# Optimization experiments

Measured on AMD Instinct MI355X. Metric: run time of the kernel, lower is better.

## Reference

```python
import jax, jax.numpy as jnp
import numpy as np
import math

TOKEN_DIM = 1024
NUM_HEADS = 16
HEAD_DIM = TOKEN_DIM // NUM_HEADS
T, B, N = 32, 32, 64


def setup_inputs() -> dict:
    key = jax.random.key(0)
    ks = jax.random.split(key, 9)
    query_vec = jax.random.normal(ks[0], (T, B, TOKEN_DIM), dtype=jnp.float32)
    tokens = jax.random.normal(ks[1], (T, B, N, TOKEN_DIM), dtype=jnp.float32)
    gate_logits = jax.random.normal(ks[2], (T, B, N), dtype=jnp.float32)
    scale = 1.0 / math.sqrt(TOKEN_DIM)
    Wq = jax.random.normal(ks[3], (TOKEN_DIM, TOKEN_DIM), dtype=jnp.float32) * scale
    Wk = jax.random.normal(ks[4], (TOKEN_DIM, TOKEN_DIM), dtype=jnp.float32) * scale
    Wv = jax.random.normal(ks[5], (TOKEN_DIM, TOKEN_DIM), dtype=jnp.float32) * scale
    bq = jnp.zeros((TOKEN_DIM,), dtype=jnp.float32)
    bk = jnp.zeros((TOKEN_DIM,), dtype=jnp.float32)
    bv = jnp.zeros((TOKEN_DIM,), dtype=jnp.float32)
    return {"query_vec": query_vec, "tokens": tokens, "gate_logits": gate_logits,
            "Wq": Wq, "bq": bq, "Wk": Wk, "bk": bk, "Wv": Wv, "bv": bv}


def reference(query_vec, tokens, gate_logits, Wq, bq, Wk, bk, Wv, bv):
    # QKV projections
    q = query_vec @ Wq + bq                      # [T,B,D]
    k = tokens @ Wk + bk                         # [T,B,N,D]
    v = tokens @ Wv + bv                         # [T,B,N,D]
    q = q.reshape(T, B, NUM_HEADS, HEAD_DIM)
    k = k.reshape(T, B, N, NUM_HEADS, HEAD_DIM)
    v = v.reshape(T, B, N, NUM_HEADS, HEAD_DIM)
    logits = jnp.einsum('tbhd,tbnhd->tbhn', q, k) / math.sqrt(HEAD_DIM)
    logits = logits + gate_logits[:, :, None, :]
    attn = jax.nn.softmax(logits, axis=-1)       # [T,B,H,N]
    attended = jnp.einsum('tbhn,tbnhd->tbhd', attn, v)
    attended = attended.reshape(T, B, TOKEN_DIM)
    mean_attn = attn.mean(axis=2)                # [T,B,N]
    return (attended, mean_attn, logits)
```

## Files before the change

### kernel.cpp

```cpp
#include <hip/hip_runtime.h>
#include <hip/hip_bf16.h>
#include <hip/hip_cooperative_groups.h>

namespace cg = cooperative_groups;

typedef __attribute__((ext_vector_type(4))) float f32x4;
typedef __attribute__((ext_vector_type(8))) short bf16x8;
typedef unsigned int u32;
typedef unsigned short u16;

#define DEV static __device__ __forceinline__


DEV u16 f2bf(float x){
  union { float f; u32 u; } v; v.f = x;
  u32 r = v.u + 0x7FFFu + ((v.u >> 16) & 1u);
  return (u16)(r >> 16);
}
DEV float bf2f(u16 s){
  union { u32 u; float f; } v; v.u = ((u32)s) << 16;
  return v.f;
}

#define MFMA16(a,b,c) __builtin_amdgcn_mfma_f32_16x16x32_bf16((a),(b),(c),0,0,0)

DEV int tok_off(int n, int dbyte){ return n*2048 + (dbyte ^ ((n & 7) << 4)); }

#define MEGA_DYN_LDS 65536

__global__ __launch_bounds__(256, 2) void k_mega(
    const float* __restrict__ qv, const float* __restrict__ tokens,
    const float* __restrict__ gate,
    const float* __restrict__ Wq, const float* __restrict__ bq,
    const float* __restrict__ Wk, const float* __restrict__ bk,
    const float* __restrict__ Wv, const float* __restrict__ bv,
    u16* __restrict__ qvB, u16* __restrict__ WqT, u16* __restrict__ WkB,
    u16* __restrict__ WvT, float* __restrict__ qf, u16* __restrict__ qb,
    u16* __restrict__ U, u16* __restrict__ ctxb,
    float* __restrict__ out_att, float* __restrict__ out_mean,
    float* __restrict__ out_logits){
  extern __shared__ __align__(16) char smem[];
  __shared__ __align__(16) char sstat[10496];
  cg::grid_group grid = cg::this_grid();
  const int tid = threadIdx.x;
  const int bx  = blockIdx.x;
  const int l = tid & 63, w = tid >> 6, g = l >> 4, li = l & 15;

  {
    const f32x4* s4 = (const f32x4*)qv;
    uint2* d2 = (uint2*)qvB;
    int g0 = bx*256 + tid;
    #pragma unroll
    for (int i = 0; i < 2; ++i){
      int idx = g0 + i*131072;
      f32x4 v = s4[idx];
      uint2 pk;
      pk.x = (u32)f2bf(v.x) | ((u32)f2bf(v.y) << 16);
      pk.y = (u32)f2bf(v.z) | ((u32)f2bf(v.w) << 16);
      d2[idx] = pk;
    }
  }
  {
    u16 (*tile)[65] = (u16 (*)[65])sstat;
    for (int tl = bx; tl < 768; tl += 512){
      __syncthreads();
      const int which = tl >> 8, t8 = tl & 255;
      const float* src = which==0 ? Wq : (which==1 ? Wk : Wv);
      const int bi = (t8 >> 4) << 6, bj = (t8 & 15) << 6;
      #pragma unroll
      for (int k2 = 0; k2 < 16; ++k2){
        int e = tid + (k2 << 8); int r = e >> 6, c = e & 63;
        tile[r][c] = f2bf(src[(size_t)(bi + r)*1024 + bj + c]);
      }
      __syncthreads();
      if (which == 1){
        #pragma unroll
        for (int k2 = 0; k2 < 16; ++k2){
          int e = tid + (k2 << 8); int r = e >> 6, c = e & 63;
          WkB[(size_t)(bi + r)*1024 + bj + c] = tile[r][c];
        }
      } else {
        u16* dst = which==0 ? WqT : WvT;
        #pragma unroll
        for (int k2 = 0; k2 < 16; ++k2){
          int e = tid + (k2 << 8); int r = e >> 6, c = e & 63;
          dst[(size_t)(bj + r)*1024 + bi + c] = tile[c][r];
        }
      }
    }
  }
  __threadfence(); grid.sync(); __threadfence();

  {
    const int wm = w & 1, wn = w >> 1;
    const int m_base = (bx >> 5)*64 + wm*32;
    const int n_base = (bx & 31)*32 + wn*16;
    f32x4 acc[2]; acc[0] = (f32x4)0.0f; acc[1] = (f32x4)0.0f;
    #pragma unroll 4
    for (int kb = 0; kb < 32; ++kb){
      const int k0 = kb*32 + g*8;
      bf16x8 b = *(const bf16x8*)(WqT + (size_t)(n_base + li)*1024 + k0);
      #pragma unroll
      for (int rt = 0; rt < 2; ++rt){
        bf16x8 a = *(const bf16x8*)(qvB + (size_t)(m_base + rt*16 + li)*1024 + k0);
        acc[rt] = MFMA16(a, b, acc[rt]);
      }
    }
    #pragma unroll
    for (int rt = 0; rt < 2; ++rt)
      #pragma unroll
      for (int r = 0; r < 4; ++r){
        int m = m_base + rt*16 + g*4 + r;
        int n = n_base + li;
        float val = acc[rt][r] + bq[n];
        qf[(size_t)m*1024 + n] = val;
        qb[(size_t)m*1024 + n] = f2bf(val);
      }
  }
  __threadfence(); grid.sync(); __threadfence();

  {
    u16 (*stile)[64] = (u16 (*)[64])sstat;
    const int wm = w & 1, wn = w >> 1;
    for (int i = 0; i < 8; ++i){
      const int tl = bx*8 + i;
      const int tb0 = (tl >> 8)*64, d0 = ((tl >> 4) & 15)*64, h = tl & 15;
      f32x4 acc[2][2];
      #pragma unroll
      for (int a0=0;a0<2;++a0)
        #pragma unroll
        for (int b0=0;b0<2;++b0) acc[a0][b0] = (f32x4)0.0f;
      #pragma unroll
      for (int kb = 0; kb < 2; ++kb){
        const int k0 = h*64 + kb*32 + g*8;
        bf16x8 a[2], b[2];
        #pragma unroll
        for (int rt=0;rt<2;++rt)
          a[rt] = *(const bf16x8*)(qb + (size_t)(tb0 + wm*32 + rt*16 + li)*1024 + k0);
        #pragma unroll
        for (int ct=0;ct<2;++ct)
          b[ct] = *(const bf16x8*)(WkB + (size_t)(d0 + wn*32 + ct*16 + li)*1024 + k0);
        #pragma unroll
        for (int rt=0;rt<2;++rt)
          #pragma unroll
          for (int ct=0;ct<2;++ct)
            acc[rt][ct] = MFMA16(a[rt], b[ct], acc[rt][ct]);
      }
      __syncthreads();
      #pragma unroll
      for (int rt=0;rt<2;++rt)
        #pragma unroll
        for (int ct=0;ct<2;++ct)
          #pragma unroll
          for (int r=0;r<4;++r)
            stile[wm*32 + rt*16 + g*4 + r][wn*32 + ct*16 + li] = f2bf(acc[rt][ct][r]);
      __syncthreads();
      const int rr = tid >> 2, cg4 = tid & 3;
      f32x4* dst = (f32x4*)(U + ((size_t)(tb0 + rr)*16 + h)*1024 + d0 + cg4*16);
      const f32x4* s4 = (const f32x4*)(&stile[rr][cg4*16]);
      dst[0] = s4[0]; dst[1] = s4[1];
    }
  }
  __threadfence(); grid.sync(); __threadfence();

  {
    float* part_s   = (float*)(sstat);
    float* logits_s = (float*)(sstat + 4096);
    float* p_s      = (float*)(sstat + 8192);
    float* csum     = (float*)(sstat + 10240);
    float* r_s      = (float*)(sstat + 10304);
    float* mzs      = (float*)(sstat + 10368);
    const int nt = w & 1, kh = w >> 1;
    const int sh = tid >> 4, sj = tid & 15;

    __syncthreads();
    for (int tbi = 0; tbi < 2; ++tbi){
      const int tb = bx + tbi*512;

      bf16x8 a[16];
      const bf16x8* Ub = (const bf16x8*)(U + (size_t)tb*16384);
      #pragma unroll
      for (int i = 0; i < 16; ++i)
        a[i] = Ub[li*128 + (kh*16 + i)*4 + g];

      {
        const float* qp = qf + (size_t)tb*1024 + sh*64 + sj*4;
        const float* bp = bk + sh*64 + sj*4;
        float part = qp[0]*bp[0] + qp[1]*bp[1] + qp[2]*bp[2] + qp[3]*bp[3];
        part += __shfl_xor(part, 1); part += __shfl_xor(part, 2);
        part += __shfl_xor(part, 4); part += __shfl_xor(part, 8);
        if (sj == 0) csum[sh] = part;
      }

      float m_run = -1e30f, z_run = 0.0f;
      f32x4 cacc[4][4];
      #pragma unroll
      for (int i=0;i<4;++i)
        #pragma unroll
        for (int j=0;j<4;++j) cacc[i][j] = (f32x4)0.0f;

      const f32x4* src4 = (const f32x4*)(tokens + (size_t)tb*65536);

      for (int c = 0; c < 2; ++c){
        const int n0 = c*32;
        __syncthreads();
        #pragma unroll 8
        for (int it = 0; it < 32; ++it){
          f32x4 v = src4[(size_t)(n0 + it)*256 + tid];
          uint2 pk;
          pk.x = (u32)f2bf(v.x) | ((u32)f2bf(v.y) << 16);
          pk.y = (u32)f2bf(v.z) | ((u32)f2bf(v.w) << 16);
          *(uint2*)(smem + tok_off(it, tid*8)) = pk;
        }
        __syncthreads();
        {
          f32x4 acc = (f32x4)0.0f;
          #pragma unroll
          for (int i = 0; i < 16; ++i){
            int kb = kh*16 + i;
            bf16x8 b = *(const bf16x8*)(smem + tok_off(nt*16 + li, (kb*32 + g*8)*2));
            acc = MFMA16(a[i], b, acc);
          }
          *(f32x4*)(part_s + (size_t)(w*64 + l)*4) = acc;
          __syncthreads();
          if (kh == 0){
            acc += *(const f32x4*)(part_s + (size_t)((w+2)*64 + l)*4);
            float gv = gate[(size_t)tb*64 + n0 + nt*16 + li];
            #pragma unroll
            for (int r = 0; r < 4; ++r){
              int h = g*4 + r;
              logits_s[h*64 + n0 + nt*16 + li] = (acc[r] + csum[h])*0.125f + gv;
            }
          }
          __syncthreads();
        }
        {
          float lv0 = logits_s[sh*64 + n0 + sj];
          float lv1 = logits_s[sh*64 + n0 + 16 + sj];
          out_logits[(size_t)tb*1024 + sh*64 + n0 + sj]      = lv0;
          out_logits[(size_t)tb*1024 + sh*64 + n0 + 16 + sj] = lv1;
          float cm = fmaxf(lv0, lv1);
          cm = fmaxf(cm, __shfl_xor(cm, 1)); cm = fmaxf(cm, __shfl_xor(cm, 2));
          cm = fmaxf(cm, __shfl_xor(cm, 4)); cm = fmaxf(cm, __shfl_xor(cm, 8));
          float m_new = fmaxf(m_run, cm);
          float rsc = __expf(m_run - m_new);
          float p0 = __expf(lv0 - m_new), p1 = __expf(lv1 - m_new);
          float zs = p0 + p1;
          zs += __shfl_xor(zs, 1); zs += __shfl_xor(zs, 2);
          zs += __shfl_xor(zs, 4); zs += __shfl_xor(zs, 8);
          z_run = z_run * rsc + zs;
          m_run = m_new;
          p_s[sj*16 + sh]        = p0;
          p_s[(sj + 16)*16 + sh] = p1;
          if (sj == 0){
            r_s[sh] = rsc;
            if (c == 1){ mzs[sh*2] = m_new; mzs[sh*2 + 1] = 1.0f / z_run; }
          }
        }
        __syncthreads();
        {
          float rr[4];
          #pragma unroll
          for (int hh = 0; hh < 4; ++hh) rr[hh] = r_s[w*4 + hh];
          #pragma unroll
          for (int dq = 0; dq < 4; ++dq)
            #pragma unroll
            for (int hh = 0; hh < 4; ++hh) cacc[dq][hh] *= rr[hh];
          for (int nl = 0; nl < 32; ++nl){
            f32x4 p = *(const f32x4*)(p_s + nl*16 + w*4);
            #pragma unroll
            for (int dq = 0; dq < 4; ++dq){
              uint2 t2 = *(const uint2*)(smem + tok_off(nl, (dq*256 + l*4)*2));
              float f0 = bf2f((u16)(t2.x & 0xFFFFu));
              float f1 = bf2f((u16)(t2.x >> 16));
              float f2 = bf2f((u16)(t2.y & 0xFFFFu));
              float f3 = bf2f((u16)(t2.y >> 16));
              #pragma unroll
              for (int hh = 0; hh < 4; ++hh){
                float av = p[hh];
                cacc[dq][hh].x += av*f0; cacc[dq][hh].y += av*f1;
                cacc[dq][hh].z += av*f2; cacc[dq][hh].w += av*f3;
              }
            }
          }
        }
      }

      if (tid < 64){
        float s = 0.0f;
        #pragma unroll
        for (int h = 0; h < 16; ++h)
          s += __expf(logits_s[h*64 + tid] - mzs[h*2]) * mzs[h*2 + 1];
        out_mean[(size_t)tb*64 + tid] = s * 0.0625f;
      }

      #pragma unroll
      for (int hh = 0; hh < 4; ++hh){
        const int h = w*4 + hh;
        const float zinv = mzs[h*2 + 1];
        #pragma unroll
        for (int dq = 0; dq < 4; ++dq){
          f32x4 v = cacc[dq][hh];
          uint2 pk;
          pk.x = (u32)f2bf(v.x * zinv) | ((u32)f2bf(v.y * zinv) << 16);
          pk.y = (u32)f2bf(v.z * zinv) | ((u32)f2bf(v.w * zinv) << 16);
          *(uint2*)(ctxb + ((size_t)tb*16 + h)*1024 + dq*256 + l*4) = pk;
        }
      }
      __syncthreads();
    }
  }
  __threadfence(); grid.sync(); __threadfence();

  {
    const int wm = w & 1, wn = w >> 1;
    const int m_base = (bx >> 4)*32, h = bx & 15;
    f32x4 acc[2]; acc[0] = (f32x4)0.0f; acc[1] = (f32x4)0.0f;
    #pragma unroll 4
    for (int kb = 0; kb < 32; ++kb){
      const int k0 = kb*32 + g*8;
      bf16x8 a = *(const bf16x8*)(ctxb + ((size_t)(m_base + wm*16 + li)*16 + h)*1024 + k0);
      #pragma unroll
      for (int ct = 0; ct < 2; ++ct){
        bf16x8 b = *(const bf16x8*)(WvT + (size_t)(h*64 + wn*32 + ct*16 + li)*1024 + k0);
        acc[ct] = MFMA16(a, b, acc[ct]);
      }
    }
    #pragma unroll
    for (int ct = 0; ct < 2; ++ct)
      #pragma unroll
      for (int r = 0; r < 4; ++r){
        int m = m_base + wm*16 + g*4 + r;
        int dout = h*64 + wn*32 + ct*16 + li;
        out_att[(size_t)m*1024 + dout] = acc[ct][r] + bv[dout];
      }
  }
}

__global__ __launch_bounds__(256) void k_convert(
    const float* __restrict__ Wq, const float* __restrict__ Wk, const float* __restrict__ Wv,
    u16* __restrict__ WqT, u16* __restrict__ WkB, u16* __restrict__ WvT){
  __shared__ u16 tile[64][65];
  const int which = blockIdx.y;
  const float* src = which==0 ? Wq : (which==1 ? Wk : Wv);
  const int bi = (blockIdx.x >> 4) << 6;
  const int bj = (blockIdx.x & 15) << 6;
  const int t  = threadIdx.x;
  #pragma unroll
  for (int k2 = 0; k2 < 16; ++k2){
    int e = t + (k2 << 8);
    int r = e >> 6, c = e & 63;
    tile[r][c] = f2bf(src[(size_t)(bi + r)*1024 + bj + c]);
  }
  __syncthreads();
  if (which == 1){
    #pragma unroll
    for (int k2 = 0; k2 < 16; ++k2){
      int e = t + (k2 << 8); int r = e >> 6, c = e & 63;
      WkB[(size_t)(bi + r)*1024 + bj + c] = tile[r][c];
    }
  } else {
    u16* dst = which==0 ? WqT : WvT;
    #pragma unroll
    for (int k2 = 0; k2 < 16; ++k2){
      int e = t + (k2 << 8); int r = e >> 6, c = e & 63;
      dst[(size_t)(bj + r)*1024 + bi + c] = tile[c][r];
    }
  }
}

__global__ __launch_bounds__(256) void k_qproj(
    const float* __restrict__ qv, const u16* __restrict__ WqT, const float* __restrict__ bq,
    float* __restrict__ qf, u16* __restrict__ qb){
  const int l = threadIdx.x & 63, w = threadIdx.x >> 6;
  const int wm = w & 1, wn = w >> 1;
  const int g = l >> 4, li = l & 15;
  const int m_base = blockIdx.x*64 + wm*32;
  const int n_base = blockIdx.y*64 + wn*32;
  f32x4 acc[2][2];
  #pragma unroll
  for (int i=0;i<2;++i)
    #pragma unroll
    for (int j=0;j<2;++j) acc[i][j] = (f32x4)0.0f;

  #pragma unroll 4
  for (int kb = 0; kb < 32; ++kb){
    const int k0 = kb*32 + g*8;
    bf16x8 a[2], b[2];
    #pragma unroll
    for (int rt = 0; rt < 2; ++rt){
      const float* p = qv + (size_t)(m_base + rt*16 + li)*1024 + k0;
      f32x4 lo = *(const f32x4*)p;
      f32x4 hi = *(const f32x4*)(p+4);
      union { u16 s[8]; bf16x8 v; } u;
      u.s[0]=f2bf(lo.x); u.s[1]=f2bf(lo.y); u.s[2]=f2bf(lo.z); u.s[3]=f2bf(lo.w);
      u.s[4]=f2bf(hi.x); u.s[5]=f2bf(hi.y); u.s[6]=f2bf(hi.z); u.s[7]=f2bf(hi.w);
      a[rt] = u.v;
    }
    #pragma unroll
    for (int ct = 0; ct < 2; ++ct)
      b[ct] = *(const bf16x8*)(WqT + (size_t)(n_base + ct*16 + li)*1024 + k0);
    #pragma unroll
    for (int rt = 0; rt < 2; ++rt)
      #pragma unroll
      for (int ct = 0; ct < 2; ++ct)
        acc[rt][ct] = MFMA16(a[rt], b[ct], acc[rt][ct]);
  }
  #pragma unroll
  for (int rt=0;rt<2;++rt)
    #pragma unroll
    for (int ct=0;ct<2;++ct)
      #pragma unroll
      for (int r=0;r<4;++r){
        int m = m_base + rt*16 + g*4 + r;
        int n = n_base + ct*16 + li;
        float val = acc[rt][ct][r] + bq[n];
        qf[(size_t)m*1024 + n] = val;
        qb[(size_t)m*1024 + n] = f2bf(val);
      }
}

__global__ __launch_bounds__(256) void k_umat(
    const u16* __restrict__ qb, const u16* __restrict__ WkB, u16* __restrict__ U){
  __shared__ __align__(16) u16 stile[64][64];
  const int l = threadIdx.x & 63, w = threadIdx.x >> 6;
  const int wm = w & 1, wn = w >> 1, g = l >> 4, li = l & 15;
  const int tb0 = blockIdx.x*64, d0 = blockIdx.y*64, h = blockIdx.z;
  f32x4 acc[2][2];
  #pragma unroll
  for (int i=0;i<2;++i)
    #pragma unroll
    for (int j=0;j<2;++j) acc[i][j] = (f32x4)0.0f;

  #pragma unroll
  for (int kb = 0; kb < 2; ++kb){
    const int k0 = h*64 + kb*32 + g*8;
    bf16x8 a[2], b[2];
    #pragma unroll
    for (int rt=0;rt<2;++rt)
      a[rt] = *(const bf16x8*)(qb + (size_t)(tb0 + wm*32 + rt*16 + li)*1024 + k0);
    #pragma unroll
    for (int ct=0;ct<2;++ct)
      b[ct] = *(const bf16x8*)(WkB + (size_t)(d0 + wn*32 + ct*16 + li)*1024 + k0);
    #pragma unroll
    for (int rt=0;rt<2;++rt)
      #pragma unroll
      for (int ct=0;ct<2;++ct)
        acc[rt][ct] = MFMA16(a[rt], b[ct], acc[rt][ct]);
  }
  #pragma unroll
  for (int rt=0;rt<2;++rt)
    #pragma unroll
    for (int ct=0;ct<2;++ct)
      #pragma unroll
      for (int r=0;r<4;++r)
        stile[wm*32 + rt*16 + g*4 + r][wn*32 + ct*16 + li] = f2bf(acc[rt][ct][r]);
  __syncthreads();
  const int r = threadIdx.x >> 2, cg4 = threadIdx.x & 3;
  f32x4* dst = (f32x4*)(U + ((size_t)(tb0 + r)*16 + h)*1024 + d0 + cg4*16);
  const f32x4* s4 = (const f32x4*)(&stile[r][cg4*16]);
  dst[0] = s4[0]; dst[1] = s4[1];
}

#define K3_LDS 76032
__global__ __launch_bounds__(256, 2) void k_attn(
    const float* __restrict__ tokens, const float* __restrict__ gate,
    const u16* __restrict__ U, const float* __restrict__ qf, const float* __restrict__ bk,
    float* __restrict__ out_logits, float* __restrict__ out_mean, u16* __restrict__ ctx){
  extern __shared__ __align__(16) char smem[];
  float* part_s   = (float*)(smem + 65536);
  float* logits_s = (float*)(smem + 69632);
  float* p_s      = (float*)(smem + 73728);
  float* csum     = (float*)(smem + 75776);
  float* r_s      = (float*)(smem + 75840);
  float* mzs      = (float*)(smem + 75904);
  const int tb = blockIdx.x;
  const int tid = threadIdx.x;
  const int l = tid & 63, w = tid >> 6, g = l >> 4, li = l & 15;
  const int nt = w & 1, kh = w >> 1;
  const int sh = tid >> 4, sj = tid & 15;

  bf16x8 a[16];
  const bf16x8* Ub = (const bf16x8*)(U + (size_t)tb*16384);
  #pragma unroll
  for (int i = 0; i < 16; ++i)
    a[i] = Ub[li*128 + (kh*16 + i)*4 + g];

  {
    const float* qp = qf + (size_t)tb*1024 + sh*64 + sj*4;
    const float* bp = bk + sh*64 + sj*4;
    float part = qp[0]*bp[0] + qp[1]*bp[1] + qp[2]*bp[2] + qp[3]*bp[3];
    part += __shfl_xor(part, 1); part += __shfl_xor(part, 2);
    part += __shfl_xor(part, 4); part += __shfl_xor(part, 8);
    if (sj == 0) csum[sh] = part;
  }

  float m_run = -1e30f, z_run = 0.0f;
  f32x4 cacc[4][4];
  #pragma unroll
  for (int i=0;i<4;++i)
    #pragma unroll
    for (int j=0;j<4;++j) cacc[i][j] = (f32x4)0.0f;

  const f32x4* src4 = (const f32x4*)(tokens + (size_t)tb*65536);

  for (int c = 0; c < 2; ++c){
    const int n0 = c*32;
    __syncthreads();
    #pragma unroll 8
    for (int it = 0; it < 32; ++it){
      f32x4 v = src4[(size_t)(n0 + it)*256 + tid];
      uint2 pk;
      pk.x = (u32)f2bf(v.x) | ((u32)f2bf(v.y) << 16);
      pk.y = (u32)f2bf(v.z) | ((u32)f2bf(v.w) << 16);
      *(uint2*)(smem + tok_off(it, tid*8)) = pk;
    }
    __syncthreads();
    {
      f32x4 acc = (f32x4)0.0f;
      #pragma unroll
      for (int i = 0; i < 16; ++i){
        int kb = kh*16 + i;
        bf16x8 b = *(const bf16x8*)(smem + tok_off(nt*16 + li, (kb*32 + g*8)*2));
        acc = MFMA16(a[i], b, acc);
      }
      *(f32x4*)(part_s + (size_t)(w*64 + l)*4) = acc;
      __syncthreads();
      if (kh == 0){
        acc += *(const f32x4*)(part_s + (size_t)((w+2)*64 + l)*4);
        float gv = gate[(size_t)tb*64 + n0 + nt*16 + li];
        #pragma unroll
        for (int r = 0; r < 4; ++r){
          int h = g*4 + r;
          logits_s[h*64 + n0 + nt*16 + li] = (acc[r] + csum[h])*0.125f + gv;
        }
      }
      __syncthreads();
    }
    {
      float lv0 = logits_s[sh*64 + n0 + sj];
      float lv1 = logits_s[sh*64 + n0 + 16 + sj];
      out_logits[(size_t)tb*1024 + sh*64 + n0 + sj]      = lv0;
      out_logits[(size_t)tb*1024 + sh*64 + n0 + 16 + sj] = lv1;
      float cm = fmaxf(lv0, lv1);
      cm = fmaxf(cm, __shfl_xor(cm, 1)); cm = fmaxf(cm, __shfl_xor(cm, 2));
      cm = fmaxf(cm, __shfl_xor(cm, 4)); cm = fmaxf(cm, __shfl_xor(cm, 8));
      float m_new = fmaxf(m_run, cm);
      float rsc = __expf(m_run - m_new);
      float p0 = __expf(lv0 - m_new), p1 = __expf(lv1 - m_new);
      float zs = p0 + p1;
      zs += __shfl_xor(zs, 1); zs += __shfl_xor(zs, 2);
      zs += __shfl_xor(zs, 4); zs += __shfl_xor(zs, 8);
      z_run = z_run * rsc + zs;
      m_run = m_new;
      p_s[sj*16 + sh]        = p0;
      p_s[(sj + 16)*16 + sh] = p1;
      if (sj == 0){
        r_s[sh] = rsc;
        if (c == 1){ mzs[sh*2] = m_new; mzs[sh*2 + 1] = 1.0f / z_run; }
      }
    }
    __syncthreads();
    {
      float rr[4];
      #pragma unroll
      for (int hh = 0; hh < 4; ++hh) rr[hh] = r_s[w*4 + hh];
      #pragma unroll
      for (int dq = 0; dq < 4; ++dq)
        #pragma unroll
        for (int hh = 0; hh < 4; ++hh) cacc[dq][hh] *= rr[hh];
      for (int nl = 0; nl < 32; ++nl){
        f32x4 p = *(const f32x4*)(p_s + nl*16 + w*4);
        #pragma unroll
        for (int dq = 0; dq < 4; ++dq){
          uint2 t2 = *(const uint2*)(smem + tok_off(nl, (dq*256 + l*4)*2));
          float f0 = bf2f((u16)(t2.x & 0xFFFFu));
          float f1 = bf2f((u16)(t2.x >> 16));
          float f2 = bf2f((u16)(t2.y & 0xFFFFu));
          float f3 = bf2f((u16)(t2.y >> 16));
          #pragma unroll
          for (int hh = 0; hh < 4; ++hh){
            float av = p[hh];
            cacc[dq][hh].x += av*f0; cacc[dq][hh].y += av*f1;
            cacc[dq][hh].z += av*f2; cacc[dq][hh].w += av*f3;
          }
        }
      }
    }
  }

  if (tid < 64){
    float s = 0.0f;
    #pragma unroll
    for (int h = 0; h < 16; ++h)
      s += __expf(logits_s[h*64 + tid] - mzs[h*2]) * mzs[h*2 + 1];
    out_mean[(size_t)tb*64 + tid] = s * 0.0625f;
  }

  #pragma unroll
  for (int hh = 0; hh < 4; ++hh){
    const int h = w*4 + hh;
    const float zinv = mzs[h*2 + 1];
    #pragma unroll
    for (int dq = 0; dq < 4; ++dq){
      f32x4 v = cacc[dq][hh];
      uint2 pk;
      pk.x = (u32)f2bf(v.x * zinv) | ((u32)f2bf(v.y * zinv) << 16);
      pk.y = (u32)f2bf(v.z * zinv) | ((u32)f2bf(v.w * zinv) << 16);
      *(uint2*)(ctx + ((size_t)tb*16 + h)*1024 + dq*256 + l*4) = pk;
    }
  }
}

__global__ __launch_bounds__(256) void k_attended(
    const u16* __restrict__ ctx, const u16* __restrict__ WvT, const float* __restrict__ bv,
    float* __restrict__ out_att){
  const int l = threadIdx.x & 63, w = threadIdx.x >> 6;
  const int wm = w & 1, wn = w >> 1, g = l >> 4, li = l & 15;
  const int tb0 = blockIdx.x*64, h = blockIdx.y;
  f32x4 acc[2][2];
  #pragma unroll
  for (int i=0;i<2;++i)
    #pragma unroll
    for (int j=0;j<2;++j) acc[i][j] = (f32x4)0.0f;

  #pragma unroll 4
  for (int kb = 0; kb < 32; ++kb){
    const int k0 = kb*32 + g*8;
    bf16x8 a[2], b[2];
    #pragma unroll
    for (int rt=0;rt<2;++rt)
      a[rt] = *(const bf16x8*)(ctx + ((size_t)(tb0 + wm*32 + rt*16 + li)*16 + h)*1024 + k0);
    #pragma unroll
    for (int ct=0;ct<2;++ct)
      b[ct] = *(const bf16x8*)(WvT + (size_t)(h*64 + wn*32 + ct*16 + li)*1024 + k0);
    #pragma unroll
    for (int rt=0;rt<2;++rt)
      #pragma unroll
      for (int ct=0;ct<2;++ct)
        acc[rt][ct] = MFMA16(a[rt], b[ct], acc[rt][ct]);
  }
  #pragma unroll
  for (int rt=0;rt<2;++rt)
    #pragma unroll
    for (int ct=0;ct<2;++ct)
      #pragma unroll
      for (int r=0;r<4;++r){
        int m = tb0 + wm*32 + rt*16 + g*4 + r;
        int dout = h*64 + wn*32 + ct*16 + li;
        out_att[(size_t)m*1024 + dout] = acc[rt][ct][r] + bv[dout];
      }
}

extern "C" void kernel_launch(void* const* d_in, const int* in_sizes, int n_in,
                              void* d_out, int out_size, void* d_ws, size_t ws_size,
                              hipStream_t stream){
  const float* qv     = (const float*)d_in[0];
  const float* tokens = (const float*)d_in[1];
  const float* gate   = (const float*)d_in[2];
  const float* Wq     = (const float*)d_in[3];
  const float* bq     = (const float*)d_in[4];
  const float* Wk     = (const float*)d_in[5];
  const float* bk     = (const float*)d_in[6];
  const float* Wv     = (const float*)d_in[7];
  const float* bv     = (const float*)d_in[8];

  char* ws = (char*)d_ws;
  u16*   qvB = (u16*)(ws);
  u16*   WqT = (u16*)(ws + (2u<<20));
  u16*   WkB = (u16*)(ws + (4u<<20));
  u16*   WvT = (u16*)(ws + (6u<<20));
  float* qf  = (float*)(ws + (8u<<20));
  u16*   qb  = (u16*)(ws + (12u<<20));
  u16*   U   = (u16*)(ws + (14u<<20));
  u16*   ctxb= (u16*)(ws + (46u<<20));

  float* out_att    = (float*)d_out;
  float* out_mean   = out_att + 1048576;
  float* out_logits = out_att + 1114112;

  int dev = 0; (void)hipGetDevice(&dev);
  int coop = 0; (void)hipDeviceGetAttribute(&coop, hipDeviceAttributeCooperativeLaunch, dev);
  int ncu = 0;  (void)hipDeviceGetAttribute(&ncu, hipDeviceAttributeMultiprocessorCount, dev);
  int perCU = 0;
  hipError_t oe = hipOccupancyMaxActiveBlocksPerMultiprocessor(
                      &perCU, (const void*)k_mega, 256, (size_t)MEGA_DYN_LDS);
  bool use_coop = (coop != 0) && (oe == hipSuccess) && ((long)perCU * (long)ncu >= 512);

  if (use_coop){
    void* args[] = { (void*)&qv, (void*)&tokens, (void*)&gate,
                     (void*)&Wq, (void*)&bq, (void*)&Wk, (void*)&bk,
                     (void*)&Wv, (void*)&bv,
                     (void*)&qvB, (void*)&WqT, (void*)&WkB, (void*)&WvT,
                     (void*)&qf, (void*)&qb, (void*)&U, (void*)&ctxb,
                     (void*)&out_att, (void*)&out_mean, (void*)&out_logits };
    hipError_t le = hipLaunchCooperativeKernel((const void*)k_mega, dim3(512), dim3(256),
                                               args, MEGA_DYN_LDS, stream);
    if (le == hipSuccess) return;
    use_coop = false;
  }

  (void)hipFuncSetAttribute((const void*)k_attn,
                            hipFuncAttributeMaxDynamicSharedMemorySize, K3_LDS);
  k_convert <<<dim3(256, 3),    256, 0,      stream>>>(Wq, Wk, Wv, WqT, WkB, WvT);
  k_qproj   <<<dim3(16, 16),    256, 0,      stream>>>(qv, WqT, bq, qf, qb);
  k_umat    <<<dim3(16, 16, 16),256, 0,      stream>>>(qb, WkB, U);
  k_attn    <<<dim3(1024),      256, K3_LDS, stream>>>(tokens, gate, U, qf, bk,
                                                       out_logits, out_mean, ctxb);
  k_attended<<<dim3(16, 16),    256, 0,      stream>>>(ctxb, WvT, bv, out_att);
}
```

Measured before the change: 177.1 us.

## Prefetch next token chunk into registers while computing softmax and context

Flattens the two-level (tb, chunk) loop in the attention phase into four rounds. Each round issues the global loads for the next 32-token chunk into a register staging array before the softmax and context accumulation, then converts it to bf16 and writes it into shared memory afterwards. The aim is to hide global-memory load latency of the token stream behind compute. The cost is 32 extra f32x4 registers of staging per thread, which may cause spills or lower occupancy in a cooperative kernel.

```diff
diff --git a/kernel.cpp b/kernel.cpp
--- a/kernel.cpp
+++ b/kernel.cpp
@@ -174,16 +174,35 @@
     const int sh = tid >> 4, sj = tid & 15;
 
     __syncthreads();
-    for (int tbi = 0; tbi < 2; ++tbi){
-      const int tb = bx + tbi*512;
-
-      bf16x8 a[16];
-      const bf16x8* Ub = (const bf16x8*)(U + (size_t)tb*16384);
-      #pragma unroll
-      for (int i = 0; i < 16; ++i)
-        a[i] = Ub[li*128 + (kh*16 + i)*4 + g];
-
-      {
+
+    {
+      const f32x4* src4 = (const f32x4*)(tokens + (size_t)bx*65536);
+      f32x4 pstg[32];
+      #pragma unroll
+      for (int it = 0; it < 32; ++it) pstg[it] = src4[(size_t)it*256 + tid];
+      #pragma unroll
+      for (int it = 0; it < 32; ++it){
+        f32x4 v = pstg[it];
+        uint2 pk;
+        pk.x = (u32)f2bf(v.x) | ((u32)f2bf(v.y) << 16);
+        pk.y = (u32)f2bf(v.z) | ((u32)f2bf(v.w) << 16);
+        *(uint2*)(smem + tok_off(it, tid*8)) = pk;
+      }
+    }
+
+    float m_run = -1e30f, z_run = 0.0f;
+    f32x4 cacc[4][4];
+
+    for (int r = 0; r < 4; ++r){
+      const int c = r & 1, n0 = c*32;
+      const int tb = bx + (r >> 1)*512;
+
+      if (c == 0){
+        m_run = -1e30f; z_run = 0.0f;
+        #pragma unroll
+        for (int i=0;i<4;++i)
+          #pragma unroll
+          for (int j=0;j<4;++j) cacc[i][j] = (f32x4)0.0f;
         const float* qp = qf + (size_t)tb*1024 + sh*64 + sj*4;
         const float* bp = bk + sh*64 + sj*4;
         float part = qp[0]*bp[0] + qp[1]*bp[1] + qp[2]*bp[2] + qp[3]*bp[3];
@@ -192,122 +211,131 @@
         if (sj == 0) csum[sh] = part;
       }
 
-      float m_run = -1e30f, z_run = 0.0f;
-      f32x4 cacc[4][4];
-      #pragma unroll
-      for (int i=0;i<4;++i)
-        #pragma unroll
-        for (int j=0;j<4;++j) cacc[i][j] = (f32x4)0.0f;
-
-      const f32x4* src4 = (const f32x4*)(tokens + (size_t)tb*65536);
-
-      for (int c = 0; c < 2; ++c){
-        const int n0 = c*32;
+      __syncthreads();
+
+      {
+        bf16x8 a[16];
+        const bf16x8* Ub = (const bf16x8*)(U + (size_t)tb*16384);
+        #pragma unroll
+        for (int i = 0; i < 16; ++i)
+          a[i] = Ub[li*128 + (kh*16 + i)*4 + g];
+        f32x4 acc = (f32x4)0.0f;
+        #pragma unroll
+        for (int i = 0; i < 16; ++i){
+          int kb = kh*16 + i;
+          bf16x8 b = *(const bf16x8*)(smem + tok_off(nt*16 + li, (kb*32 + g*8)*2));
+          acc = MFMA16(a[i], b, acc);
+        }
+        *(f32x4*)(part_s + (size_t)(w*64 + l)*4) = acc;
         __syncthreads();
-        #pragma unroll 8
+        if (kh == 0){
+          acc += *(const f32x4*)(part_s + (size_t)((w+2)*64 + l)*4);
+          float gv = gate[(size_t)tb*64 + n0 + nt*16 + li];
+          #pragma unroll
+          for (int rg = 0; rg < 4; ++rg){
+            int h = g*4 + rg;
+            logits_s[h*64 + n0 + nt*16 + li] = (acc[rg] + csum[h])*0.125f + gv;
+          }
+        }
+        __syncthreads();
+      }
+
+      f32x4 stg[32];
+      const int rn = r + 1;
+      if (rn < 4){
+        const f32x4* srcn = (const f32x4*)(tokens + (size_t)(bx + (rn >> 1)*512)*65536);
+        const int n0n = (rn & 1)*32;
+        #pragma unroll
+        for (int it = 0; it < 32; ++it)
+          stg[it] = srcn[(size_t)(n0n + it)*256 + tid];
+      }
+
+      {
+        float lv0 = logits_s[sh*64 + n0 + sj];
+        float lv1 = logits_s[sh*64 + n0 + 16 + sj];
+        out_logits[(size_t)tb*1024 + sh*64 + n0 + sj]      = lv0;
+        out_logits[(size_t)tb*1024 + sh*64 + n0 + 16 + sj] = lv1;
+        float cm = fmaxf(lv0, lv1);
+        cm = fmaxf(cm, __shfl_xor(cm, 1)); cm = fmaxf(cm, __shfl_xor(cm, 2));
+        cm = fmaxf(cm, __shfl_xor(cm, 4)); cm = fmaxf(cm, __shfl_xor(cm, 8));
+        float m_new = fmaxf(m_run, cm);
+        float rsc = __expf(m_run - m_new);
+        float p0 = __expf(lv0 - m_new), p1 = __expf(lv1 - m_new);
+        float zs = p0 + p1;
+        zs += __shfl_xor(zs, 1); zs += __shfl_xor(zs, 2);
+        zs += __shfl_xor(zs, 4); zs += __shfl_xor(zs, 8);
+        z_run = z_run * rsc + zs;
+        m_run = m_new;
+        p_s[sj*16 + sh]        = p0;
+        p_s[(sj + 16)*16 + sh] = p1;
+        if (sj == 0){
+          r_s[sh] = rsc;
+          if (c == 1){ mzs[sh*2] = m_new; mzs[sh*2 + 1] = 1.0f / z_run; }
+        }
+      }
+      __syncthreads();
+
+      {
+        float rr[4];
+        #pragma unroll
+        for (int hh = 0; hh < 4; ++hh) rr[hh] = r_s[w*4 + hh];
+        #pragma unroll
+        for (int dq = 0; dq < 4; ++dq)
+          #pragma unroll
+          for (int hh = 0; hh < 4; ++hh) cacc[dq][hh] *= rr[hh];
+        for (int nl = 0; nl < 32; ++nl){
+          f32x4 p = *(const f32x4*)(p_s + nl*16 + w*4);
+          #pragma unroll
+          for (int dq = 0; dq < 4; ++dq){
+            uint2 t2 = *(const uint2*)(smem + tok_off(nl, (dq*256 + l*4)*2));
+            float f0 = bf2f((u16)(t2.x & 0xFFFFu));
+            float f1 = bf2f((u16)(t2.x >> 16));
+            float f2 = bf2f((u16)(t2.y & 0xFFFFu));
+            float f3 = bf2f((u16)(t2.y >> 16));
+            #pragma unroll
+            for (int hh = 0; hh < 4; ++hh){
+              float av = p[hh];
+              cacc[dq][hh].x += av*f0; cacc[dq][hh].y += av*f1;
+              cacc[dq][hh].z += av*f2; cacc[dq][hh].w += av*f3;
+            }
+          }
+        }
+      }
+      __syncthreads();
+
+      if (rn < 4){
+        #pragma unroll
         for (int it = 0; it < 32; ++it){
-          f32x4 v = src4[(size_t)(n0 + it)*256 + tid];
+          f32x4 v = stg[it];
           uint2 pk;
           pk.x = (u32)f2bf(v.x) | ((u32)f2bf(v.y) << 16);
           pk.y = (u32)f2bf(v.z) | ((u32)f2bf(v.w) << 16);
           *(uint2*)(smem + tok_off(it, tid*8)) = pk;
         }
-        __syncthreads();
-        {
-          f32x4 acc = (f32x4)0.0f;
-          #pragma unroll
-          for (int i = 0; i < 16; ++i){
-            int kb = kh*16 + i;
-            bf16x8 b = *(const bf16x8*)(smem + tok_off(nt*16 + li, (kb*32 + g*8)*2));
-            acc = MFMA16(a[i], b, acc);
+      }
+
+      if (c == 1){
+        if (tid < 64){
+          float s = 0.0f;
+          #pragma unroll
+          for (int h = 0; h < 16; ++h)
+            s += __expf(logits_s[h*64 + tid] - mzs[h*2]) * mzs[h*2 + 1];
+          out_mean[(size_t)tb*64 + tid] = s * 0.0625f;
+        }
+        #pragma unroll
+        for (int hh = 0; hh < 4; ++hh){
+          const int h = w*4 + hh;
+          const float zinv = mzs[h*2 + 1];
+          #pragma unroll
+          for (int dq = 0; dq < 4; ++dq){
+            f32x4 v = cacc[dq][hh];
+            uint2 pk;
+            pk.x = (u32)f2bf(v.x * zinv) | ((u32)f2bf(v.y * zinv) << 16);
+            pk.y = (u32)f2bf(v.z * zinv) | ((u32)f2bf(v.w * zinv) << 16);
+            *(uint2*)(ctxb + ((size_t)tb*16 + h)*1024 + dq*256 + l*4) = pk;
           }
-          *(f32x4*)(part_s + (size_t)(w*64 + l)*4) = acc;
-          __syncthreads();
-          if (kh == 0){
-            acc += *(const f32x4*)(part_s + (size_t)((w+2)*64 + l)*4);
-            float gv = gate[(size_t)tb*64 + n0 + nt*16 + li];
-            #pragma unroll
-            for (int r = 0; r < 4; ++r){
-              int h = g*4 + r;
-              logits_s[h*64 + n0 + nt*16 + li] = (acc[r] + csum[h])*0.125f + gv;
-            }
-          }
-          __syncthreads();
-        }
-        {
-          float lv0 = logits_s[sh*64 + n0 + sj];
-          float lv1 = logits_s[sh*64 + n0 + 16 + sj];
-          out_logits[(size_t)tb*1024 + sh*64 + n0 + sj]      = lv0;
-          out_logits[(size_t)tb*1024 + sh*64 + n0 + 16 + sj] = lv1;
-          float cm = fmaxf(lv0, lv1);
-          cm = fmaxf(cm, __shfl_xor(cm, 1)); cm = fmaxf(cm, __shfl_xor(cm, 2));
-          cm = fmaxf(cm, __shfl_xor(cm, 4)); cm = fmaxf(cm, __shfl_xor(cm, 8));
-          float m_new = fmaxf(m_run, cm);
-          float rsc = __expf(m_run - m_new);
-          float p0 = __expf(lv0 - m_new), p1 = __expf(lv1 - m_new);
-          float zs = p0 + p1;
-          zs += __shfl_xor(zs, 1); zs += __shfl_xor(zs, 2);
-          zs += __shfl_xor(zs, 4); zs += __shfl_xor(zs, 8);
-          z_run = z_run * rsc + zs;
-          m_run = m_new;
-          p_s[sj*16 + sh]        = p0;
-          p_s[(sj + 16)*16 + sh] = p1;
-          if (sj == 0){
-            r_s[sh] = rsc;
-            if (c == 1){ mzs[sh*2] = m_new; mzs[sh*2 + 1] = 1.0f / z_run; }
-          }
-        }
-        __syncthreads();
-        {
-          float rr[4];
-          #pragma unroll
-          for (int hh = 0; hh < 4; ++hh) rr[hh] = r_s[w*4 + hh];
-          #pragma unroll
-          for (int dq = 0; dq < 4; ++dq)
-            #pragma unroll
-            for (int hh = 0; hh < 4; ++hh) cacc[dq][hh] *= rr[hh];
-          for (int nl = 0; nl < 32; ++nl){
-            f32x4 p = *(const f32x4*)(p_s + nl*16 + w*4);
-            #pragma unroll
-            for (int dq = 0; dq < 4; ++dq){
-              uint2 t2 = *(const uint2*)(smem + tok_off(nl, (dq*256 + l*4)*2));
-              float f0 = bf2f((u16)(t2.x & 0xFFFFu));
-              float f1 = bf2f((u16)(t2.x >> 16));
-              float f2 = bf2f((u16)(t2.y & 0xFFFFu));
-              float f3 = bf2f((u16)(t2.y >> 16));
-              #pragma unroll
-              for (int hh = 0; hh < 4; ++hh){
-                float av = p[hh];
-                cacc[dq][hh].x += av*f0; cacc[dq][hh].y += av*f1;
-                cacc[dq][hh].z += av*f2; cacc[dq][hh].w += av*f3;
-              }
-            }
-          }
-        }
-      }
-
-      if (tid < 64){
-        float s = 0.0f;
-        #pragma unroll
-        for (int h = 0; h < 16; ++h)
-          s += __expf(logits_s[h*64 + tid] - mzs[h*2]) * mzs[h*2 + 1];
-        out_mean[(size_t)tb*64 + tid] = s * 0.0625f;
-      }
-
-      #pragma unroll
-      for (int hh = 0; hh < 4; ++hh){
-        const int h = w*4 + hh;
-        const float zinv = mzs[h*2 + 1];
-        #pragma unroll
-        for (int dq = 0; dq < 4; ++dq){
-          f32x4 v = cacc[dq][hh];
-          uint2 pk;
-          pk.x = (u32)f2bf(v.x * zinv) | ((u32)f2bf(v.y * zinv) << 16);
-          pk.y = (u32)f2bf(v.z * zinv) | ((u32)f2bf(v.w * zinv) << 16);
-          *(uint2*)(ctxb + ((size_t)tb*16 + h)*1024 + dq*256 + l*4) = pk;
-        }
-      }
-      __syncthreads();
+        }
+      }
     }
   }
   __threadfence(); grid.sync(); __threadfence();
```

Result: no change. 174.8 us (-1.3%).
